# Optimization experiments

Hardware: AMD Instinct MI355X
Metric: run time of the kernel (lower is better)

## Reference

```python
import jax, jax.numpy as jnp
import numpy as np
import math

B, S, D, H = 4, 2048, 1024, 16
HD = D // H

def setup_inputs() -> dict:
    key = jax.random.key(0)
    k = jax.random.split(key, 5)
    scale = 1.0 / math.sqrt(D)
    return {
        "x": jax.random.normal(k[0], (B, S, D), dtype=jnp.float32),
        "W_qkv": jax.random.normal(k[1], (D, 3 * D), dtype=jnp.float32) * scale,
        "b_qkv": jnp.zeros((3 * D,), dtype=jnp.float32),
        "W_out": jax.random.normal(k[2], (D, D), dtype=jnp.float32) * scale,
        "b_out": jnp.zeros((D,), dtype=jnp.float32),
    }

def reference(x, W_qkv, b_qkv, W_out, b_out):
    b, s, d = x.shape
    qkv = x @ W_qkv + b_qkv                       # [b, s, 3d]
    qkv = qkv.reshape(b, s, 3, H, HD)
    q, k, v = jnp.moveaxis(qkv, 2, 0)             # each [b, s, H, HD]
    q = jnp.transpose(q, (0, 2, 1, 3))            # [b, H, s, hd]
    k = jnp.transpose(k, (0, 2, 1, 3))
    v = jnp.transpose(v, (0, 2, 1, 3))
    scores = jnp.einsum('bhqd,bhkd->bhqk', q, k) / math.sqrt(HD)
    causal = jnp.tril(jnp.ones((s, s), dtype=bool))
    scores = jnp.where(causal, scores, -jnp.inf)
    weights = jax.nn.softmax(scores, axis=-1)     # dropout = identity (eval)
    attended = jnp.einsum('bhqk,bhkd->bhqd', weights, v)
    attended = jnp.transpose(attended, (0, 2, 1, 3)).reshape(b, s, d)
    return attended @ W_out + b_out
```

## Files before the change

### kernel.cpp

```cpp
#include <hip/hip_runtime.h>
#include <hip/hip_bf16.h>

typedef __attribute__((ext_vector_type(4))) float f32x4;
typedef __attribute__((ext_vector_type(16))) float f32x16;
typedef __attribute__((ext_vector_type(8))) short short8;

static constexpr int Ssz = 2048;
static constexpr int Dsz = 1024;

__device__ __forceinline__ unsigned short f2bf(float f){
  union { float f; unsigned u; } c; c.f = f;
  unsigned r = c.u + 0x7fffu + ((c.u >> 16) & 1u);
  return (unsigned short)(r >> 16);
}

__device__ __forceinline__ void gl2lds16(const void* g, void* l){
  __builtin_amdgcn_global_load_lds(
    (const __attribute__((address_space(1))) unsigned int*)g,
    (__attribute__((address_space(3))) unsigned int*)l, 16, 0, 0);
}

__device__ __forceinline__ unsigned cvtpk(float lo, float hi){
  unsigned r;
  asm("v_cvt_pk_bf16_f32 %0, %1, %2" : "=v"(r) : "v"(lo), "v"(hi));
  return r;
}

__device__ __forceinline__ void permswap(unsigned &a, unsigned &b){
  asm volatile("v_permlane32_swap_b32 %0, %1" : "+v"(a), "+v"(b));
}

__device__ __forceinline__ float xmax64(float x){
  float a = x, b;
  asm volatile("v_mov_b32 %0, %1" : "=v"(b) : "v"(a));
  asm volatile("v_permlane32_swap_b32 %0, %1" : "+v"(a), "+v"(b));
  return fmaxf(a, b);
}
__device__ __forceinline__ float xsum64(float x){
  float a = x, b;
  asm volatile("v_mov_b32 %0, %1" : "=v"(b) : "v"(a));
  asm volatile("v_permlane32_swap_b32 %0, %1" : "+v"(a), "+v"(b));
  return a + b;
}

__global__ void cvt_kernel(const float* __restrict__ in, unsigned short* __restrict__ out, int n){
  int i = (blockIdx.x * 256 + threadIdx.x) * 8;
  if (i >= n) return;
  float4 a = *(const float4*)(in + i);
  float4 b = *(const float4*)(in + i + 4);
  short8 o;
  o[0]=(short)f2bf(a.x); o[1]=(short)f2bf(a.y); o[2]=(short)f2bf(a.z); o[3]=(short)f2bf(a.w);
  o[4]=(short)f2bf(b.x); o[5]=(short)f2bf(b.y); o[6]=(short)f2bf(b.z); o[7]=(short)f2bf(b.w);
  *(short8*)(out + i) = o;
}

__global__ void transpose_kernel(const float* __restrict__ in, unsigned short* __restrict__ out,
                                 int R, int C){
  __shared__ float tile[32][33];
  int c0 = blockIdx.x * 32, r0 = blockIdx.y * 32;
  int tx = threadIdx.x, ty = threadIdx.y;
  #pragma unroll
  for (int k = 0; k < 4; ++k)
    tile[ty + 8*k][tx] = in[(size_t)(r0 + ty + 8*k) * C + c0 + tx];
  __syncthreads();
  #pragma unroll
  for (int k = 0; k < 4; ++k)
    out[(size_t)(c0 + ty + 8*k) * R + r0 + tx] = f2bf(tile[tx][ty + 8*k]);
}

#define BM 128
#define BN 128
#define BKg 64

__global__ __launch_bounds__(256, 2)
void gemm_bt(const unsigned short* __restrict__ A, const unsigned short* __restrict__ Bt,
             int M, int N, int K,
             const float* __restrict__ bias, int mode,
             unsigned short* __restrict__ Qp, unsigned short* __restrict__ Kp,
             unsigned short* __restrict__ Vtp, float* __restrict__ Out)
{
  __shared__ unsigned short ldsA[BM * BKg];
  __shared__ unsigned short ldsB[BN * BKg];
  const int tid = threadIdx.x;
  const int wid = tid >> 6;
  const int lane = tid & 63;
  const int lr = lane & 15, lg = lane >> 4;
  const int wr = wid >> 1, wc = wid & 1;
  const int m0 = blockIdx.y * BM, n0 = blockIdx.x * BN;

  const f32x4 vzero = {0.f, 0.f, 0.f, 0.f};
  f32x4 acc[4][4];
  #pragma unroll
  for (int i = 0; i < 4; ++i)
    #pragma unroll
    for (int j = 0; j < 4; ++j) acc[i][j] = vzero;

  for (int k0 = 0; k0 < K; k0 += BKg){
    __syncthreads();
    #pragma unroll
    for (int it = 0; it < 4; ++it){
      int c = it * 256 + tid;
      int row = c >> 3;
      int sc = (c & 7) ^ (row & 7);
      gl2lds16(A  + (size_t)(m0 + row) * K + k0 + sc * 8,
               (char*)ldsA + (it * 256 + wid * 64) * 16);
      gl2lds16(Bt + (size_t)(n0 + row) * K + k0 + sc * 8,
               (char*)ldsB + (it * 256 + wid * 64) * 16);
    }
    __syncthreads();
    #pragma unroll
    for (int kc = 0; kc < 2; ++kc){
      short8 af[4], bfr[4];
      #pragma unroll
      for (int i = 0; i < 4; ++i){
        int row = wr * 64 + i * 16 + lr;
        int off = row * 128 + lg * 16 + kc * 64;
        off ^= (row & 7) << 4;
        af[i] = *(const short8*)((const char*)ldsA + off);
      }
      #pragma unroll
      for (int j = 0; j < 4; ++j){
        int row = wc * 64 + j * 16 + lr;
        int off = row * 128 + lg * 16 + kc * 64;
        off ^= (row & 7) << 4;
        bfr[j] = *(const short8*)((const char*)ldsB + off);
      }
      #pragma unroll
      for (int i = 0; i < 4; ++i)
        #pragma unroll
        for (int j = 0; j < 4; ++j)
          acc[i][j] = __builtin_amdgcn_mfma_f32_16x16x32_bf16(af[i], bfr[j], acc[i][j], 0, 0, 0);
    }
  }

  if (mode == 0){
    const float qscale = 0.125f * 1.4426950408889634f;
    #pragma unroll
    for (int i = 0; i < 4; ++i)
      #pragma unroll
      for (int j = 0; j < 4; ++j)
        #pragma unroll
        for (int r = 0; r < 4; ++r){
          int gm = m0 + wr * 64 + i * 16 + lg * 4 + r;
          int gn = n0 + wc * 64 + j * 16 + lr;
          float v = acc[i][j][r] + bias[gn];
          int which = gn >> 10;
          int h = (gn >> 6) & 15;
          int hd = gn & 63;
          int b = gm >> 11;
          int s = gm & 2047;
          size_t bh = (size_t)(b * 16 + h);
          if (which == 0)      Qp[(bh * Ssz + s) * 64 + hd] = f2bf(v * qscale);
          else if (which == 1) Kp[(bh * Ssz + s) * 64 + hd] = f2bf(v);
          else                 Vtp[(bh * 64 + hd) * Ssz + s] = f2bf(v);
        }
  } else {
    #pragma unroll
    for (int i = 0; i < 4; ++i)
      #pragma unroll
      for (int j = 0; j < 4; ++j)
        #pragma unroll
        for (int r = 0; r < 4; ++r){
          int gm = m0 + wr * 64 + i * 16 + lg * 4 + r;
          int gn = n0 + wc * 64 + j * 16 + lr;
          Out[(size_t)gm * N + gn] = acc[i][j][r] + bias[gn];
        }
  }
}

__global__ __launch_bounds__(256, 2)
void attn_kernel(const unsigned short* __restrict__ Qp, const unsigned short* __restrict__ Kp,
                 const unsigned short* __restrict__ Vtp, unsigned short* __restrict__ Att)
{
  __shared__ unsigned short ldsK[2][4096];
  __shared__ unsigned short ldsV[2][4096];
  const int tid = threadIdx.x;
  const int wid = tid >> 6;
  const int lane = tid & 63;
  const int lq = lane & 31;
  const int hi = lane >> 5;
  const int bh = blockIdx.y;
  const int b = bh >> 4, hh = bh & 15;

  #pragma unroll 1
  for (int job = 0; job < 2; ++job){
    const int qt = job ? (15 - (int)blockIdx.x) : (int)blockIdx.x;
    const int q0w = qt * 128 + wid * 32;
    const int qa = q0w + lq;
    const int nt = 2 * qt + 2;

    short8 qf[4];
    {
      const unsigned short* Qb = Qp + ((size_t)bh * Ssz + q0w + lq) * 64 + hi * 8;
      #pragma unroll
      for (int ks = 0; ks < 4; ++ks) qf[ks] = *(const short8*)(Qb + ks * 16);
    }

    f32x16 Ot[2];
    #pragma unroll
    for (int d = 0; d < 2; ++d)
      #pragma unroll
      for (int r = 0; r < 16; ++r) Ot[d][r] = 0.f;
    float mrun = -3e38f, lsum = 0.f;

    #pragma unroll
    for (int it = 0; it < 2; ++it){
      int c = it * 256 + tid;
      int row = c >> 3, sc = (c & 7) ^ (row & 7);
      gl2lds16(Kp  + ((size_t)bh * Ssz + row) * 64 + sc * 8,
               (char*)&ldsK[0][0] + (it * 256 + wid * 64) * 16);
      gl2lds16(Vtp + ((size_t)bh * 64 + row) * Ssz + sc * 8,
               (char*)&ldsV[0][0] + (it * 256 + wid * 64) * 16);
    }
    __syncthreads();

    for (int kt = 0; kt < nt; ++kt){
      const int cur = kt & 1;
      if (kt + 1 < nt){
        const int nxt = cur ^ 1;
        #pragma unroll
        for (int it = 0; it < 2; ++it){
          int c = it * 256 + tid;
          int row = c >> 3, sc = (c & 7) ^ (row & 7);
          gl2lds16(Kp  + ((size_t)bh * Ssz + (kt + 1) * 64 + row) * 64 + sc * 8,
                   (char*)&ldsK[nxt][0] + (it * 256 + wid * 64) * 16);
          gl2lds16(Vtp + ((size_t)bh * 64 + row) * Ssz + (kt + 1) * 64 + sc * 8,
                   (char*)&ldsV[nxt][0] + (it * 256 + wid * 64) * 16);
        }
      }

      if (kt * 64 <= q0w + 31){
        const char* Kb = (const char*)&ldsK[cur][0];
        const char* Vb = (const char*)&ldsV[cur][0];

        f32x16 S[2];
        #pragma unroll
        for (int kb = 0; kb < 2; ++kb)
          #pragma unroll
          for (int r = 0; r < 16; ++r) S[kb][r] = 0.f;
        #pragma unroll
        for (int ks = 0; ks < 4; ++ks){
          int col = 32 * ks + 16 * hi;
          int r0 = lq, r1 = 32 + lq;
          short8 k0 = *(const short8*)(Kb + ((r0 * 128 + col) ^ ((r0 & 7) << 4)));
          short8 k1 = *(const short8*)(Kb + ((r1 * 128 + col) ^ ((r1 & 7) << 4)));
          S[0] = __builtin_amdgcn_mfma_f32_32x32x16_bf16(k0, qf[ks], S[0], 0, 0, 0);
          S[1] = __builtin_amdgcn_mfma_f32_32x32x16_bf16(k1, qf[ks], S[1], 0, 0, 0);
        }

        if (kt * 64 + 63 > q0w){
          #pragma unroll
          for (int r = 0; r < 16; ++r){
            int keyb = kt * 64 + (r & 3) + ((r >> 2) << 3) + 4 * hi;
            if (keyb > qa)      S[0][r] = -3e38f;
            if (keyb + 32 > qa) S[1][r] = -3e38f;
          }
        }

        float t16[16];
        #pragma unroll
        for (int r = 0; r < 16; ++r) t16[r] = fmaxf(S[0][r], S[1][r]);
        float t8[8];
        #pragma unroll
        for (int r = 0; r < 8; ++r) t8[r] = fmaxf(t16[r], t16[r + 8]);
        float t4[4];
        #pragma unroll
        for (int r = 0; r < 4; ++r) t4[r] = fmaxf(t8[r], t8[r + 4]);
        float pmax = fmaxf(fmaxf(t4[0], t4[1]), fmaxf(t4[2], t4[3]));
        pmax = xmax64(pmax);

        if (!__all(pmax - mrun <= 8.0f)){
          float mn = fmaxf(mrun, pmax);
          float scl = __builtin_amdgcn_exp2f(mrun - mn);
          mrun = mn;
          lsum *= scl;
          #pragma unroll
          for (int d = 0; d < 2; ++d)
            #pragma unroll
            for (int r = 0; r < 16; ++r) Ot[d][r] *= scl;
        }

        #pragma unroll
        for (int kb = 0; kb < 2; ++kb)
          #pragma unroll
          for (int r = 0; r < 16; ++r)
            S[kb][r] = __builtin_amdgcn_exp2f(S[kb][r] - mrun);

        #pragma unroll
        for (int r = 0; r < 16; ++r) t16[r] = S[0][r] + S[1][r];
        #pragma unroll
        for (int r = 0; r < 8; ++r) t8[r] = t16[r] + t16[r + 8];
        #pragma unroll
        for (int r = 0; r < 4; ++r) t4[r] = t8[r] + t8[r + 4];
        float psum = (t4[0] + t4[1]) + (t4[2] + t4[3]);
        psum = xsum64(psum);
        lsum += psum;

        #pragma unroll
        for (int s = 0; s < 4; ++s){
          const int sb = s >> 1, s1 = s & 1;
          unsigned u0 = cvtpk(S[sb][8 * s1 + 0], S[sb][8 * s1 + 1]);
          unsigned u1 = cvtpk(S[sb][8 * s1 + 2], S[sb][8 * s1 + 3]);
          unsigned u2 = cvtpk(S[sb][8 * s1 + 4], S[sb][8 * s1 + 5]);
          unsigned u3 = cvtpk(S[sb][8 * s1 + 6], S[sb][8 * s1 + 7]);
          permswap(u0, u2);
          permswap(u1, u3);
          union { unsigned u[4]; short8 s8; } pb;
          pb.u[0] = u0; pb.u[1] = u1; pb.u[2] = u2; pb.u[3] = u3;

          int col = 32 * s + 16 * hi;
          int r0 = lq, r1 = 32 + lq;
          short8 v0 = *(const short8*)(Vb + ((r0 * 128 + col) ^ ((r0 & 7) << 4)));
          short8 v1 = *(const short8*)(Vb + ((r1 * 128 + col) ^ ((r1 & 7) << 4)));
          Ot[0] = __builtin_amdgcn_mfma_f32_32x32x16_bf16(v0, pb.s8, Ot[0], 0, 0, 0);
          Ot[1] = __builtin_amdgcn_mfma_f32_32x32x16_bf16(v1, pb.s8, Ot[1], 0, 0, 0);
        }
      }
      __syncthreads();
    }

    float inv = 1.0f / lsum;
    unsigned short* ep = &ldsK[0][0] + wid * 2048;
    #pragma unroll
    for (int d = 0; d < 2; ++d)
      #pragma unroll
      for (int g = 0; g < 4; ++g)
        #pragma unroll
        for (int cp = 0; cp < 2; ++cp){
          int r = g * 4 + cp * 2;
          unsigned w = cvtpk(Ot[d][r] * inv, Ot[d][r + 1] * inv);
          int dd = d * 32 + g * 8 + 4 * hi + cp * 2;
          int byte = lq * 128 + ((dd * 2) ^ ((lq & 7) << 4));
          *(unsigned*)((char*)ep + byte) = w;
        }
    __syncthreads();
    #pragma unroll
    for (int i = 0; i < 4; ++i){
      int qr = i * 8 + (lane >> 3);
      int cc = lane & 7;
      int byte = qr * 128 + ((cc * 16) ^ ((qr & 7) << 4));
      short8 vv = *(const short8*)((const char*)ep + byte);
      *(short8*)(Att + ((size_t)(b * Ssz + q0w + qr)) * Dsz + hh * 64 + cc * 8) = vv;
    }
    __syncthreads();
  }
}

extern "C" void kernel_launch(void* const* d_in, const int* in_sizes, int n_in,
                              void* d_out, int out_size, void* d_ws, size_t ws_size,
                              hipStream_t stream) {
  const float* x    = (const float*)d_in[0];
  const float* Wqkv = (const float*)d_in[1];
  const float* bqkv = (const float*)d_in[2];
  const float* Wout = (const float*)d_in[3];
  const float* bout = (const float*)d_in[4];
  float* out = (float*)d_out;

  unsigned short* xb    = (unsigned short*)d_ws;
  unsigned short* wqkvT = xb    + (size_t)8192 * 1024;
  unsigned short* woutT = wqkvT + (size_t)3072 * 1024;
  unsigned short* Qb    = woutT + (size_t)1024 * 1024;
  unsigned short* Kb    = Qb    + (size_t)8388608;
  unsigned short* Vtb   = Kb    + (size_t)8388608;
  unsigned short* Attb  = Vtb   + (size_t)8388608;

  cvt_kernel<<<4096, 256, 0, stream>>>(x, xb, 8388608);
  transpose_kernel<<<dim3(96, 32), dim3(32, 8), 0, stream>>>(Wqkv, wqkvT, 1024, 3072);
  transpose_kernel<<<dim3(32, 32), dim3(32, 8), 0, stream>>>(Wout, woutT, 1024, 1024);
  gemm_bt<<<dim3(24, 64), 256, 0, stream>>>(xb, wqkvT, 8192, 3072, 1024,
                                            bqkv, 0, Qb, Kb, Vtb, nullptr);
  attn_kernel<<<dim3(8, 64), 256, 0, stream>>>(Qb, Kb, Vtb, Attb);
  gemm_bt<<<dim3(8, 64), 256, 0, stream>>>(Attb, woutT, 8192, 1024, 1024,
                                           bout, 1, nullptr, nullptr, nullptr, out);
}
```

Baseline: 183.9 us.

## Add dedicated 256x256 pipelined QKV GEMM with double-buffered direct-to-LDS loads

Replaces the generic 128x128 GEMM for the QKV projection with a specialized 512-thread kernel using 256x256 tiles. It double-buffers LDS, streams global-to-LDS loads in quarter-tile stages interleaved with MFMA phases, raises wave priority around MFMA bursts, and swizzles block order for L2 locality. The larger tile gives more data reuse per load, at the cost of heavier register and LDS use, and it relies on hand-placed waitcnt and barriers that must be exactly right. The output GEMM loses its mode branch.

```diff
diff --git a/kernel.cpp b/kernel.cpp
--- a/kernel.cpp
+++ b/kernel.cpp
@@ -68,6 +68,196 @@
     out[(size_t)(c0 + ty + 8*k) * R + r0 + tx] = f2bf(tile[tx][ty + 8*k]);
 }
 
+__global__ __launch_bounds__(512, 2)
+void gemm_qkv(const unsigned short* __restrict__ A, const unsigned short* __restrict__ Bt,
+              const float* __restrict__ bias,
+              unsigned short* __restrict__ Qp, unsigned short* __restrict__ Kp,
+              unsigned short* __restrict__ Vtp)
+{
+  constexpr int K = 1024, NT = 16;
+  __shared__ unsigned short ldsA[2][256 * 64];
+  __shared__ unsigned short ldsB[2][256 * 64];
+  const int tid = threadIdx.x;
+  const int wid = tid >> 6, lane = tid & 63;
+  const int lr = lane & 15, lg = lane >> 4;
+  const int wm = wid >> 2, wn = wid & 3;
+
+  int bid = blockIdx.x;
+  int swz = (bid & 7) * 48 + (bid >> 3);
+  const int m0 = (swz / 12) * 256, n0 = (swz % 12) * 256;
+
+  const f32x4 vzero = {0.f, 0.f, 0.f, 0.f};
+  f32x4 acc[8][4];
+  #pragma unroll
+  for (int i = 0; i < 8; ++i)
+    #pragma unroll
+    for (int j = 0; j < 4; ++j) acc[i][j] = vzero;
+
+  auto stage = [&](int sigma){
+    if (sigma >= 4 * NT) return;
+    const int ts = sigma >> 2, ss = sigma & 3;
+    const int buf = ts & 1;
+    #pragma unroll
+    for (int call = 0; call < 2; ++call){
+      int c = call * 512 + tid;
+      int rw = c >> 3, cc = c & 7;
+      if (ss == 0 || ss == 3){
+        int row = ((rw >> 5) << 6) + (rw & 31) + (ss == 3 ? 32 : 0);
+        int sc = cc ^ (row & 7);
+        gl2lds16(Bt + (size_t)(n0 + row) * K + ts * 64 + sc * 8,
+                 &ldsB[buf][row * 64 + cc * 8]);
+      } else {
+        int row = ((rw >> 6) << 7) + (rw & 63) + (ss == 2 ? 64 : 0);
+        int sc = cc ^ (row & 7);
+        gl2lds16(A + (size_t)(m0 + row) * K + ts * 64 + sc * 8,
+                 &ldsA[buf][row * 64 + cc * 8]);
+      }
+    }
+  };
+
+  short8 af[4][2], bf2[2][2];
+
+  stage(0); stage(1); stage(2); stage(3); stage(4);
+  asm volatile("s_waitcnt vmcnt(6)" ::: "memory");
+  __builtin_amdgcn_sched_barrier(0);
+  __builtin_amdgcn_s_barrier();
+
+  #pragma unroll 1
+  for (int t = 0; t < NT; ++t){
+    const char* baA = (const char*)&ldsA[t & 1][0];
+    const char* baB = (const char*)&ldsB[t & 1][0];
+
+    #pragma unroll
+    for (int ii = 0; ii < 4; ++ii)
+      #pragma unroll
+      for (int kk = 0; kk < 2; ++kk){
+        int row = wm * 128 + ii * 16 + lr;
+        int off = (row * 128 + lg * 16 + kk * 64) ^ ((row & 7) << 4);
+        af[ii][kk] = *(const short8*)(baA + off);
+      }
+    #pragma unroll
+    for (int jj = 0; jj < 2; ++jj)
+      #pragma unroll
+      for (int kk = 0; kk < 2; ++kk){
+        int row = wn * 64 + jj * 16 + lr;
+        int off = (row * 128 + lg * 16 + kk * 64) ^ ((row & 7) << 4);
+        bf2[jj][kk] = *(const short8*)(baB + off);
+      }
+    stage(4 * t + 5);
+    __builtin_amdgcn_s_barrier();
+    asm volatile("s_waitcnt lgkmcnt(0)" ::: "memory");
+    __builtin_amdgcn_sched_barrier(0);
+    __builtin_amdgcn_s_setprio(1);
+    #pragma unroll
+    for (int ii = 0; ii < 4; ++ii)
+      #pragma unroll
+      for (int jj = 0; jj < 2; ++jj)
+        #pragma unroll
+        for (int kk = 0; kk < 2; ++kk)
+          acc[ii][jj] = __builtin_amdgcn_mfma_f32_16x16x32_bf16(af[ii][kk], bf2[jj][kk], acc[ii][jj], 0, 0, 0);
+    __builtin_amdgcn_s_setprio(0);
+    asm volatile("s_waitcnt vmcnt(6)" ::: "memory");
+    __builtin_amdgcn_sched_barrier(0);
+    __builtin_amdgcn_s_barrier();
+
+    #pragma unroll
+    for (int ii = 0; ii < 4; ++ii)
+      #pragma unroll
+      for (int kk = 0; kk < 2; ++kk){
+        int row = wm * 128 + 64 + ii * 16 + lr;
+        int off = (row * 128 + lg * 16 + kk * 64) ^ ((row & 7) << 4);
+        af[ii][kk] = *(const short8*)(baA + off);
+      }
+    stage(4 * t + 6);
+    __builtin_amdgcn_s_barrier();
+    asm volatile("s_waitcnt lgkmcnt(0)" ::: "memory");
+    __builtin_amdgcn_sched_barrier(0);
+    __builtin_amdgcn_s_setprio(1);
+    #pragma unroll
+    for (int ii = 0; ii < 4; ++ii)
+      #pragma unroll
+      for (int jj = 0; jj < 2; ++jj)
+        #pragma unroll
+        for (int kk = 0; kk < 2; ++kk)
+          acc[4 + ii][jj] = __builtin_amdgcn_mfma_f32_16x16x32_bf16(af[ii][kk], bf2[jj][kk], acc[4 + ii][jj], 0, 0, 0);
+    __builtin_amdgcn_s_setprio(0);
+    asm volatile("s_waitcnt vmcnt(6)" ::: "memory");
+    __builtin_amdgcn_sched_barrier(0);
+    __builtin_amdgcn_s_barrier();
+
+    #pragma unroll
+    for (int jj = 0; jj < 2; ++jj)
+      #pragma unroll
+      for (int kk = 0; kk < 2; ++kk){
+        int row = wn * 64 + 32 + jj * 16 + lr;
+        int off = (row * 128 + lg * 16 + kk * 64) ^ ((row & 7) << 4);
+        bf2[jj][kk] = *(const short8*)(baB + off);
+      }
+    stage(4 * t + 7);
+    __builtin_amdgcn_s_barrier();
+    asm volatile("s_waitcnt lgkmcnt(0)" ::: "memory");
+    __builtin_amdgcn_sched_barrier(0);
+    __builtin_amdgcn_s_setprio(1);
+    #pragma unroll
+    for (int ii = 0; ii < 4; ++ii)
+      #pragma unroll
+      for (int jj = 0; jj < 2; ++jj)
+        #pragma unroll
+        for (int kk = 0; kk < 2; ++kk)
+          acc[4 + ii][2 + jj] = __builtin_amdgcn_mfma_f32_16x16x32_bf16(af[ii][kk], bf2[jj][kk], acc[4 + ii][2 + jj], 0, 0, 0);
+    __builtin_amdgcn_s_setprio(0);
+    __builtin_amdgcn_s_barrier();
+
+    #pragma unroll
+    for (int ii = 0; ii < 4; ++ii)
+      #pragma unroll
+      for (int kk = 0; kk < 2; ++kk){
+        int row = wm * 128 + ii * 16 + lr;
+        int off = (row * 128 + lg * 16 + kk * 64) ^ ((row & 7) << 4);
+        af[ii][kk] = *(const short8*)(baA + off);
+      }
+    stage(4 * t + 8);
+    __builtin_amdgcn_s_barrier();
+    asm volatile("s_waitcnt lgkmcnt(0)" ::: "memory");
+    __builtin_amdgcn_sched_barrier(0);
+    __builtin_amdgcn_s_setprio(1);
+    #pragma unroll
+    for (int ii = 0; ii < 4; ++ii)
+      #pragma unroll
+      for (int jj = 0; jj < 2; ++jj)
+        #pragma unroll
+        for (int kk = 0; kk < 2; ++kk)
+          acc[ii][2 + jj] = __builtin_amdgcn_mfma_f32_16x16x32_bf16(af[ii][kk], bf2[jj][kk], acc[ii][2 + jj], 0, 0, 0);
+    __builtin_amdgcn_s_setprio(0);
+    asm volatile("s_waitcnt vmcnt(6)" ::: "memory");
+    __builtin_amdgcn_sched_barrier(0);
+    __builtin_amdgcn_s_barrier();
+  }
+
+  asm volatile("s_waitcnt vmcnt(0)" ::: "memory");
+
+  const float qscale = 0.125f * 1.4426950408889634f;
+  #pragma unroll
+  for (int i = 0; i < 8; ++i)
+    #pragma unroll
+    for (int j = 0; j < 4; ++j)
+      #pragma unroll
+      for (int r = 0; r < 4; ++r){
+        int gm = m0 + wm * 128 + i * 16 + lg * 4 + r;
+        int gn = n0 + wn * 64 + j * 16 + lr;
+        float v = acc[i][j][r] + bias[gn];
+        int which = gn >> 10;
+        int h = (gn >> 6) & 15;
+        int hd = gn & 63;
+        int b = gm >> 11;
+        int s = gm & 2047;
+        size_t bh = (size_t)(b * 16 + h);
+        if (which == 0)      Qp[(bh * Ssz + s) * 64 + hd] = f2bf(v * qscale);
+        else if (which == 1) Kp[(bh * Ssz + s) * 64 + hd] = f2bf(v);
+        else                 Vtp[(bh * 64 + hd) * Ssz + s] = f2bf(v);
+      }
+}
+
 #define BM 128
 #define BN 128
 #define BKg 64
@@ -75,9 +265,7 @@
 __global__ __launch_bounds__(256, 2)
 void gemm_bt(const unsigned short* __restrict__ A, const unsigned short* __restrict__ Bt,
              int M, int N, int K,
-             const float* __restrict__ bias, int mode,
-             unsigned short* __restrict__ Qp, unsigned short* __restrict__ Kp,
-             unsigned short* __restrict__ Vtp, float* __restrict__ Out)
+             const float* __restrict__ bias, float* __restrict__ Out)
 {
   __shared__ unsigned short ldsA[BM * BKg];
   __shared__ unsigned short ldsB[BN * BKg];
@@ -133,39 +321,16 @@
     }
   }
 
-  if (mode == 0){
-    const float qscale = 0.125f * 1.4426950408889634f;
-    #pragma unroll
-    for (int i = 0; i < 4; ++i)
-      #pragma unroll
-      for (int j = 0; j < 4; ++j)
-        #pragma unroll
-        for (int r = 0; r < 4; ++r){
-          int gm = m0 + wr * 64 + i * 16 + lg * 4 + r;
-          int gn = n0 + wc * 64 + j * 16 + lr;
-          float v = acc[i][j][r] + bias[gn];
-          int which = gn >> 10;
-          int h = (gn >> 6) & 15;
-          int hd = gn & 63;
-          int b = gm >> 11;
-          int s = gm & 2047;
-          size_t bh = (size_t)(b * 16 + h);
-          if (which == 0)      Qp[(bh * Ssz + s) * 64 + hd] = f2bf(v * qscale);
-          else if (which == 1) Kp[(bh * Ssz + s) * 64 + hd] = f2bf(v);
-          else                 Vtp[(bh * 64 + hd) * Ssz + s] = f2bf(v);
-        }
-  } else {
-    #pragma unroll
-    for (int i = 0; i < 4; ++i)
-      #pragma unroll
-      for (int j = 0; j < 4; ++j)
-        #pragma unroll
-        for (int r = 0; r < 4; ++r){
-          int gm = m0 + wr * 64 + i * 16 + lg * 4 + r;
-          int gn = n0 + wc * 64 + j * 16 + lr;
-          Out[(size_t)gm * N + gn] = acc[i][j][r] + bias[gn];
-        }
-  }
+  #pragma unroll
+  for (int i = 0; i < 4; ++i)
+    #pragma unroll
+    for (int j = 0; j < 4; ++j)
+      #pragma unroll
+      for (int r = 0; r < 4; ++r){
+        int gm = m0 + wr * 64 + i * 16 + lg * 4 + r;
+        int gn = n0 + wc * 64 + j * 16 + lr;
+        Out[(size_t)gm * N + gn] = acc[i][j][r] + bias[gn];
+      }
 }
 
 __global__ __launch_bounds__(256, 2)
@@ -367,9 +532,7 @@
   cvt_kernel<<<4096, 256, 0, stream>>>(x, xb, 8388608);
   transpose_kernel<<<dim3(96, 32), dim3(32, 8), 0, stream>>>(Wqkv, wqkvT, 1024, 3072);
   transpose_kernel<<<dim3(32, 32), dim3(32, 8), 0, stream>>>(Wout, woutT, 1024, 1024);
-  gemm_bt<<<dim3(24, 64), 256, 0, stream>>>(xb, wqkvT, 8192, 3072, 1024,
-                                            bqkv, 0, Qb, Kb, Vtb, nullptr);
+  gemm_qkv<<<384, 512, 0, stream>>>(xb, wqkvT, bqkv, Qb, Kb, Vtb);
   attn_kernel<<<dim3(8, 64), 256, 0, stream>>>(Qb, Kb, Vtb, Attb);
-  gemm_bt<<<dim3(8, 64), 256, 0, stream>>>(Attb, woutT, 8192, 1024, 1024,
-                                           bout, 1, nullptr, nullptr, nullptr, out);
-}
+  gemm_bt<<<dim3(8, 64), 256, 0, stream>>>(Attb, woutT, 8192, 1024, 1024, bout, out);
+}
```

Result: slower. 199.9 us (+8.7%).
